# Kernel optimization log

Hardware: AMD Instinct MI355X
Metric: run time of the kernel (lower is better)

Reference implementation:

```python
import jax, jax.numpy as jnp
import numpy as np

N_HEAD = 16
N_BLOCKS = 2
EPS = 1e-6

def _rmsnorm(x, g):
    return x * jax.lax.rsqrt(jnp.mean(x * x, axis=-1, keepdims=True) + EPS) * g

def _causal_sa(x, Wqkv, Wproj, g):
    # x: (B, T, C); fused qkv, RMSNorm on q/k over full C before head split
    B, T, C = x.shape
    hd = C // N_HEAD
    q, k, v = jnp.split(x @ Wqkv, 3, axis=-1)
    q = _rmsnorm(q, g)
    k = _rmsnorm(k, g)
    def heads(t):
        return t.reshape(B, T, N_HEAD, hd).transpose(0, 2, 1, 3)
    q, k, v = heads(q), heads(k), heads(v)
    scores = jnp.einsum('bhqd,bhkd->bhqk', q, k) * (1.0 / np.sqrt(hd))
    mask = jnp.tril(jnp.ones((T, T), dtype=bool))
    scores = jnp.where(mask, scores, -jnp.finfo(scores.dtype).max)
    att = jax.nn.softmax(scores, axis=-1)
    y = jnp.einsum('bhqk,bhkd->bhqd', att, v)
    y = y.transpose(0, 2, 1, 3).reshape(B, T, C)
    return y @ Wproj

def setup_inputs() -> dict:
    key = jax.random.key(0)
    ks = jax.random.split(key, 8)
    B, ng, T, C = 2, 8, 256, 1024
    M_loc, M_glob = 16, 16
    s = 0.02
    return {
        'x': jax.random.normal(ks[0], (B, ng, T, C), jnp.float32),
        'mem_tokens': jax.random.normal(ks[1], (B, M_glob, C), jnp.float32),
        'local_mem': jax.random.normal(ks[2], (B, ng, M_loc, C), jnp.float32),
        'Wqkv_loc': jax.random.normal(ks[3], (N_BLOCKS, C, 3 * C), jnp.float32) * s,
        'Wproj_loc': jax.random.normal(ks[4], (N_BLOCKS, C, C), jnp.float32) * s,
        'g_loc': jnp.ones((N_BLOCKS, C), jnp.float32),
        'Wqkv_glob': jax.random.normal(ks[5], (N_BLOCKS, C, 3 * C), jnp.float32) * s,
        'Wproj_glob': jax.random.normal(ks[6], (N_BLOCKS, C, C), jnp.float32) * s,
        'g_glob': jnp.ones((N_BLOCKS, C), jnp.float32),
    }

def reference(x, mem_tokens, local_mem, Wqkv_loc, Wproj_loc, g_loc, Wqkv_glob, Wproj_glob, g_glob):
    B, ng, T, C = x.shape
    M_loc = local_mem.shape[2]
    M_glob = mem_tokens.shape[1]
    for i in range(N_BLOCKS):
        # local causal SA: per-group, with local mem tokens prepended
        xl = jnp.concatenate([local_mem, x], axis=2).reshape(B * ng, M_loc + T, C)
        yl = _causal_sa(xl, Wqkv_loc[i], Wproj_loc[i], g_loc[i])
        yl = yl.reshape(B, ng, M_loc + T, C)
        local_mem = yl[:, :, :M_loc, :]
        x = yl[:, :, M_loc:, :]
        # global causal SA over flattened sequence with global mem tokens
        xg = x.reshape(B, ng * T, C)
        xg = jnp.concatenate([mem_tokens, xg], axis=1)
        yg = _causal_sa(xg, Wqkv_glob[i], Wproj_glob[i], g_glob[i])
        mem_tokens = yg[:, :M_glob, :]
        x = yg[:, M_glob:, :].reshape(B, ng, T, C)
    return x
```

## Files before the change

kernel.cpp:

```cpp
#include <hip/hip_runtime.h>
#include <hip/hip_bf16.h>
#include <math.h>

typedef __attribute__((ext_vector_type(8))) short s16x8;
typedef __attribute__((ext_vector_type(4))) short s16x4;
typedef __attribute__((ext_vector_type(4))) float f32x4;

#define MPAD 4352
#define LG 2064
#define CT 8

__device__ __forceinline__ short f2b(float f) {
  unsigned u = __float_as_uint(f);
  unsigned r = (u + 0x7fffu + ((u >> 16) & 1u)) >> 16;
  return (short)(unsigned short)r;
}
__device__ __forceinline__ float b2f(short s) {
  return __uint_as_float(((unsigned)(unsigned short)s) << 16);
}

__device__ __forceinline__ void gl_lds16(const short* g, short* l) {
  __builtin_amdgcn_global_load_lds((const __attribute__((address_space(1))) short*)g,
                                   (__attribute__((address_space(3))) short*)l, 16, 0, 0);
}

__global__ __launch_bounds__(256) void transpose_cast(const float* __restrict__ in,
                                                      short* __restrict__ out,
                                                      int K, int N) {
  __shared__ float tile[32][33];
  int bn = blockIdx.x * 32;
  int bk = blockIdx.y * 32;
  for (int i = threadIdx.y; i < 32; i += 8)
    tile[i][threadIdx.x] = in[(size_t)(bk + i) * N + bn + threadIdx.x];
  __syncthreads();
  for (int i = threadIdx.y; i < 32; i += 8)
    out[(size_t)(bn + i) * K + bk + threadIdx.x] = f2b(tile[threadIdx.x][i]);
}

__global__ __launch_bounds__(256) void transpose_v(const short* __restrict__ QKV,
                                                   short* __restrict__ Vt,
                                                   int L, int Lpad) {
  __shared__ short tile[32][33];
  int sh = blockIdx.z;
  int s = sh >> 4, h = sh & 15;
  int kb = blockIdx.x * 32;
  int cb = blockIdx.y * 32;
  int tx = threadIdx.x;
  for (int i = threadIdx.y; i < 32; i += 8) {
    int key = kb + i;
    if (key > L - 1) key = L - 1;
    tile[i][tx] = QKV[(size_t)(s * L + key) * 3072 + 2048 + h * 64 + cb + tx];
  }
  __syncthreads();
  for (int i = threadIdx.y; i < 32; i += 8)
    Vt[((size_t)sh * 64 + cb + i) * Lpad + kb + tx] = tile[tx][i];
}

__global__ __launch_bounds__(256) void gemm_bt2(const short* __restrict__ A,
                                                const short* __restrict__ BT,
                                                short* __restrict__ C,
                                                int K, int N) {
  __shared__ short As[128 * 32];
  __shared__ short Bs[128 * 32];
  const int tid = threadIdx.x;
  const int lane = tid & 63;
  const int w = tid >> 6;
  const int wr = (w >> 1) * 64, wc = (w & 1) * 64;
  const int m0 = blockIdx.y * 128;
  const int n0 = blockIdx.x * 128;
  const int l15 = lane & 15, lhi = lane >> 4;

  f32x4 acc[4][4] = {};

  for (int k0 = 0; k0 < K; k0 += 32) {
    __syncthreads();
#pragma unroll
    for (int p = 0; p < 2; ++p) {
      int g = w * 128 + p * 64 + lane;
      int row = g >> 2;
      int cs = (g & 3) * 8;
      gl_lds16(A + (size_t)(m0 + row) * K + k0 + cs, &As[g * 8]);
      gl_lds16(BT + (size_t)(n0 + row) * K + k0 + cs, &Bs[g * 8]);
    }
    __syncthreads();
    s16x8 af[4], bf[4];
#pragma unroll
    for (int m = 0; m < 4; ++m)
      af[m] = *(const s16x8*)(&As[(wr + m * 16 + l15) * 32 + lhi * 8]);
#pragma unroll
    for (int n = 0; n < 4; ++n)
      bf[n] = *(const s16x8*)(&Bs[(wc + n * 16 + l15) * 32 + lhi * 8]);
#pragma unroll
    for (int m = 0; m < 4; ++m)
#pragma unroll
      for (int n = 0; n < 4; ++n)
        acc[m][n] = __builtin_amdgcn_mfma_f32_16x16x32_bf16(af[m], bf[n], acc[m][n], 0, 0, 0);
  }
#pragma unroll
  for (int m = 0; m < 4; ++m) {
    int row_base = m0 + wr + m * 16 + lhi * 4;
#pragma unroll
    for (int n = 0; n < 4; ++n) {
      int col = n0 + wc + n * 16 + l15;
#pragma unroll
      for (int r = 0; r < 4; ++r)
        C[(size_t)(row_base + r) * N + col] = f2b(acc[m][n][r]);
    }
  }
}

__global__ __launch_bounds__(256) void rmsnorm_qk(short* __restrict__ QKV,
                                                  const float* __restrict__ g) {
  int row = blockIdx.x;
  int which = blockIdx.y;
  size_t base = (size_t)row * 3072 + (size_t)which * 1024;
  int t = threadIdx.x;
  s16x4 in = *(const s16x4*)(QKV + base + t * 4);
  float v[4];
  float ss = 0.f;
#pragma unroll
  for (int j = 0; j < 4; ++j) {
    v[j] = b2f(in[j]);
    ss += v[j] * v[j];
  }
#pragma unroll
  for (int m = 32; m >= 1; m >>= 1) ss += __shfl_xor(ss, m);
  __shared__ float red[4];
  if ((t & 63) == 0) red[t >> 6] = ss;
  __syncthreads();
  float tot = red[0] + red[1] + red[2] + red[3];
  float inv = rsqrtf(tot * (1.0f / 1024.0f) + 1e-6f);
  if (which == 0) inv *= 0.125f;
  s16x4 out;
#pragma unroll
  for (int j = 0; j < 4; ++j) out[j] = f2b(v[j] * inv * g[t * 4 + j]);
  *(s16x4*)(&QKV[base + t * 4]) = out;
}

__global__ __launch_bounds__(256) void attn_causal3(const short* __restrict__ QKV,
                                                    const short* __restrict__ Vt,
                                                    short* __restrict__ Y,
                                                    int L, int Lpad) {
  const int h = blockIdx.y, s = blockIdx.z;
  const int q0 = blockIdx.x * 64;
  const int tid = threadIdx.x;
  const int lane = tid & 63, w = tid >> 6;
  const int l15 = lane & 15, lhi = lane >> 4;
  const int row0 = s * L;

  __shared__ short Ks[64][72];
  __shared__ short Vs[2][64][72];
  __shared__ short Ps[4][16][72];

  int qld = q0 + w * 16 + l15;
  if (qld > L - 1) qld = L - 1;
  const size_t qrow = (size_t)(row0 + qld) * 3072 + h * 64;
  s16x8 qf0 = *(const s16x8*)(QKV + qrow + lhi * 8);
  s16x8 qf1 = *(const s16x8*)(QKV + qrow + 32 + lhi * 8);

  float lsum[4] = {0.f, 0.f, 0.f, 0.f};
  f32x4 o[4];
#pragma unroll
  for (int d = 0; d < 4; ++d) o[d] = f32x4{0.f, 0.f, 0.f, 0.f};

  const short* Vbase = Vt + (size_t)(s * 16 + h) * 64 * Lpad;

  s16x8 kreg[2], vreg[2];
#pragma unroll
  for (int p = 0; p < 2; ++p) {
    int g = tid + p * 256;
    int kr = g >> 3, cs = (g & 7) * 8;
    int krow = kr;
    if (krow > L - 1) krow = L - 1;
    kreg[p] = *(const s16x8*)(QKV + (size_t)(row0 + krow) * 3072 + 1024 + h * 64 + cs);
    vreg[p] = *(const s16x8*)(Vbase + (size_t)kr * Lpad + cs);
  }

  int buf = 0;
  for (int kb = 0; kb <= q0; kb += 64, buf ^= 1) {
#pragma unroll
    for (int p = 0; p < 2; ++p) {
      int g = tid + p * 256;
      int kr = g >> 3, cs = (g & 7) * 8;
      *(s16x8*)(&Ks[kr][cs]) = kreg[p];
      *(s16x8*)(&Vs[buf][kr][cs]) = vreg[p];
    }
    if (kb + 64 <= q0) {
#pragma unroll
      for (int p = 0; p < 2; ++p) {
        int g = tid + p * 256;
        int kr = g >> 3, cs = (g & 7) * 8;
        int krow = kb + 64 + kr;
        if (krow > L - 1) krow = L - 1;
        kreg[p] = *(const s16x8*)(QKV + (size_t)(row0 + krow) * 3072 + 1024 + h * 64 + cs);
        vreg[p] = *(const s16x8*)(Vbase + (size_t)kr * Lpad + kb + 64 + cs);
      }
    }
    __syncthreads();

    f32x4 st[4];
#pragma unroll
    for (int n = 0; n < 4; ++n) {
      s16x8 k0 = *(const s16x8*)(&Ks[n * 16 + l15][lhi * 8]);
      s16x8 k1 = *(const s16x8*)(&Ks[n * 16 + l15][32 + lhi * 8]);
      f32x4 sa = f32x4{0.f, 0.f, 0.f, 0.f};
      sa = __builtin_amdgcn_mfma_f32_16x16x32_bf16(qf0, k0, sa, 0, 0, 0);
      sa = __builtin_amdgcn_mfma_f32_16x16x32_bf16(qf1, k1, sa, 0, 0, 0);
      st[n] = sa;
    }

    if (kb == q0) {
#pragma unroll
      for (int n = 0; n < 4; ++n) {
        int key = kb + n * 16 + l15;
#pragma unroll
        for (int r = 0; r < 4; ++r) {
          int qr = q0 + w * 16 + lhi * 4 + r;
          if (key > qr) st[n][r] = -1e30f;
        }
      }
    }

#pragma unroll
    for (int n = 0; n < 4; ++n) {
#pragma unroll
      for (int r = 0; r < 4; ++r) {
        float p = __expf(st[n][r] - 8.0f);
        Ps[w][lhi * 4 + r][n * 16 + l15] = f2b(p);
        lsum[r] += p;
      }
    }
    __syncthreads();

#pragma unroll
    for (int kk = 0; kk < 2; ++kk) {
      s16x8 pa = *(const s16x8*)(&Ps[w][l15][kk * 32 + lhi * 8]);
#pragma unroll
      for (int d = 0; d < 4; ++d) {
        s16x8 vf = *(const s16x8*)(&Vs[buf][d * 16 + l15][kk * 32 + lhi * 8]);
        o[d] = __builtin_amdgcn_mfma_f32_16x16x32_bf16(pa, vf, o[d], 0, 0, 0);
      }
    }
  }

#pragma unroll
  for (int r = 0; r < 4; ++r) {
#pragma unroll
    for (int mm = 1; mm <= 8; mm <<= 1) lsum[r] += __shfl_xor(lsum[r], mm, 16);
  }
#pragma unroll
  for (int d = 0; d < 4; ++d) {
#pragma unroll
    for (int r = 0; r < 4; ++r) {
      int qr = q0 + w * 16 + lhi * 4 + r;
      if (qr < L)
        Y[(size_t)(row0 + qr) * 1024 + h * 64 + d * 16 + l15] = f2b(o[d][r] / lsum[r]);
    }
  }
}

__global__ __launch_bounds__(256) void attn_split(const short* __restrict__ QKV,
                                                  const short* __restrict__ Vt,
                                                  float* __restrict__ o_acc,
                                                  float* __restrict__ ls_acc) {
  const int qb = blockIdx.x;
  const int chunk = blockIdx.y;
  const int sh = blockIdx.z;
  const int t0 = chunk * CT;
  if (t0 > qb) return;
  const int t1 = min(t0 + CT, qb + 1);
  const int h = sh & 15, s = sh >> 4;
  const int q0 = qb * 64;
  const int tid = threadIdx.x;
  const int lane = tid & 63, w = tid >> 6;
  const int l15 = lane & 15, lhi = lane >> 4;
  const int row0 = s * LG;
  const int Lpad = 2112;

  __shared__ short Ks[64][72];
  __shared__ short Vs[2][64][72];
  __shared__ short Ps[4][16][72];

  int qld = q0 + w * 16 + l15;
  if (qld > LG - 1) qld = LG - 1;
  const size_t qrow = (size_t)(row0 + qld) * 3072 + h * 64;
  s16x8 qf0 = *(const s16x8*)(QKV + qrow + lhi * 8);
  s16x8 qf1 = *(const s16x8*)(QKV + qrow + 32 + lhi * 8);

  float lsum[4] = {0.f, 0.f, 0.f, 0.f};
  f32x4 o[4];
#pragma unroll
  for (int d = 0; d < 4; ++d) o[d] = f32x4{0.f, 0.f, 0.f, 0.f};

  const short* Vbase = Vt + (size_t)sh * 64 * Lpad;

  s16x8 kreg[2], vreg[2];
  const int kb0 = t0 * 64;
#pragma unroll
  for (int p = 0; p < 2; ++p) {
    int g = tid + p * 256;
    int kr = g >> 3, cs = (g & 7) * 8;
    int krow = kb0 + kr;
    if (krow > LG - 1) krow = LG - 1;
    kreg[p] = *(const s16x8*)(QKV + (size_t)(row0 + krow) * 3072 + 1024 + h * 64 + cs);
    vreg[p] = *(const s16x8*)(Vbase + (size_t)kr * Lpad + kb0 + cs);
  }

  int buf = 0;
  for (int t = t0; t < t1; ++t, buf ^= 1) {
    const int kb = t * 64;
#pragma unroll
    for (int p = 0; p < 2; ++p) {
      int g = tid + p * 256;
      int kr = g >> 3, cs = (g & 7) * 8;
      *(s16x8*)(&Ks[kr][cs]) = kreg[p];
      *(s16x8*)(&Vs[buf][kr][cs]) = vreg[p];
    }
    if (t + 1 < t1) {
#pragma unroll
      for (int p = 0; p < 2; ++p) {
        int g = tid + p * 256;
        int kr = g >> 3, cs = (g & 7) * 8;
        int krow = kb + 64 + kr;
        if (krow > LG - 1) krow = LG - 1;
        kreg[p] = *(const s16x8*)(QKV + (size_t)(row0 + krow) * 3072 + 1024 + h * 64 + cs);
        vreg[p] = *(const s16x8*)(Vbase + (size_t)kr * Lpad + kb + 64 + cs);
      }
    }
    __syncthreads();

    f32x4 st[4];
#pragma unroll
    for (int n = 0; n < 4; ++n) {
      s16x8 k0 = *(const s16x8*)(&Ks[n * 16 + l15][lhi * 8]);
      s16x8 k1 = *(const s16x8*)(&Ks[n * 16 + l15][32 + lhi * 8]);
      f32x4 sa = f32x4{0.f, 0.f, 0.f, 0.f};
      sa = __builtin_amdgcn_mfma_f32_16x16x32_bf16(qf0, k0, sa, 0, 0, 0);
      sa = __builtin_amdgcn_mfma_f32_16x16x32_bf16(qf1, k1, sa, 0, 0, 0);
      st[n] = sa;
    }

    if (t == qb) {
#pragma unroll
      for (int n = 0; n < 4; ++n) {
        int key = kb + n * 16 + l15;
#pragma unroll
        for (int r = 0; r < 4; ++r) {
          int qr = q0 + w * 16 + lhi * 4 + r;
          if (key > qr) st[n][r] = -1e30f;
        }
      }
    }

#pragma unroll
    for (int n = 0; n < 4; ++n) {
#pragma unroll
      for (int r = 0; r < 4; ++r) {
        float p = __expf(st[n][r] - 8.0f);
        Ps[w][lhi * 4 + r][n * 16 + l15] = f2b(p);
        lsum[r] += p;
      }
    }
    __syncthreads();

#pragma unroll
    for (int kk = 0; kk < 2; ++kk) {
      s16x8 pa = *(const s16x8*)(&Ps[w][l15][kk * 32 + lhi * 8]);
#pragma unroll
      for (int d = 0; d < 4; ++d) {
        s16x8 vf = *(const s16x8*)(&Vs[buf][d * 16 + l15][kk * 32 + lhi * 8]);
        o[d] = __builtin_amdgcn_mfma_f32_16x16x32_bf16(pa, vf, o[d], 0, 0, 0);
      }
    }
  }

#pragma unroll
  for (int r = 0; r < 4; ++r) {
#pragma unroll
    for (int mm = 1; mm <= 8; mm <<= 1) lsum[r] += __shfl_xor(lsum[r], mm, 16);
  }
#pragma unroll
  for (int r = 0; r < 4; ++r) {
    int qr = q0 + w * 16 + lhi * 4 + r;
    if (qr < LG) {
      if (l15 == 0) atomicAdd(&ls_acc[(size_t)sh * LG + qr], lsum[r]);
#pragma unroll
      for (int d = 0; d < 4; ++d)
        atomicAdd(&o_acc[((size_t)sh * LG + qr) * 64 + d * 16 + l15], o[d][r]);
    }
  }
}

__global__ __launch_bounds__(256) void attn_merge(const float* __restrict__ o_acc,
                                                  const float* __restrict__ ls_acc,
                                                  short* __restrict__ Y) {
  int sh = blockIdx.z * 16 + blockIdx.y;
  int s = sh >> 4, h = sh & 15;
  int row = blockIdx.x * 4 + (threadIdx.x >> 6);
  int col = threadIdx.x & 63;
  if (row < LG) {
    float inv = 1.0f / ls_acc[(size_t)sh * LG + row];
    float v = o_acc[((size_t)sh * LG + row) * 64 + col];
    Y[(size_t)(s * LG + row) * 1024 + h * 64 + col] = f2b(v * inv);
  }
}

__global__ __launch_bounds__(256) void build_xl(const float* __restrict__ x,
                                                const float* __restrict__ lm,
                                                short* __restrict__ Xin) {
  int row = blockIdx.x;
  int s = row / 272, r = row % 272;
  const float* src = (r < 16) ? lm + ((size_t)s * 16 + r) * 1024
                              : x + ((size_t)s * 256 + (r - 16)) * 1024;
  int t = threadIdx.x;
  f32x4 v = *(const f32x4*)(src + t * 4);
  s16x4 o;
#pragma unroll
  for (int j = 0; j < 4; ++j) o[j] = f2b(v[j]);
  *(s16x4*)(&Xin[(size_t)row * 1024 + t * 4]) = o;
}

__global__ __launch_bounds__(256) void build_xg(const float* __restrict__ x,
                                                const float* __restrict__ mem,
                                                short* __restrict__ Xin) {
  int row = blockIdx.x;
  int sr = row < 4128 ? row : 4127;
  int b = sr / 2064, r = sr % 2064;
  const float* src = (r < 16) ? mem + ((size_t)b * 16 + r) * 1024
                              : x + ((size_t)b * 2048 + (r - 16)) * 1024;
  int t = threadIdx.x;
  f32x4 v = *(const f32x4*)(src + t * 4);
  s16x4 o;
#pragma unroll
  for (int j = 0; j < 4; ++j) o[j] = f2b(v[j]);
  *(s16x4*)(&Xin[(size_t)row * 1024 + t * 4]) = o;
}

__global__ __launch_bounds__(256) void split_local(const short* __restrict__ Pout,
                                                   float* __restrict__ x,
                                                   float* __restrict__ lm) {
  int row = blockIdx.x;
  int s = row / 272, r = row % 272;
  int t = threadIdx.x;
  s16x4 v = *(const s16x4*)(Pout + (size_t)row * 1024 + t * 4);
  float* dst = (r < 16) ? lm + ((size_t)s * 16 + r) * 1024
                        : x + ((size_t)s * 256 + (r - 16)) * 1024;
  f32x4 o;
#pragma unroll
  for (int j = 0; j < 4; ++j) o[j] = b2f(v[j]);
  *(f32x4*)(dst + t * 4) = o;
}

__global__ __launch_bounds__(256) void split_global(const short* __restrict__ Pout,
                                                    float* __restrict__ x,
                                                    float* __restrict__ mem) {
  int row = blockIdx.x;
  int b = row / 2064, r = row % 2064;
  int t = threadIdx.x;
  s16x4 v = *(const s16x4*)(Pout + (size_t)row * 1024 + t * 4);
  float* dst = (r < 16) ? mem + ((size_t)b * 16 + r) * 1024
                        : x + ((size_t)b * 2048 + (r - 16)) * 1024;
  f32x4 o;
#pragma unroll
  for (int j = 0; j < 4; ++j) o[j] = b2f(v[j]);
  *(f32x4*)(dst + t * 4) = o;
}

extern "C" void kernel_launch(void* const* d_in, const int* in_sizes, int n_in,
                              void* d_out, int out_size, void* d_ws, size_t ws_size,
                              hipStream_t stream) {
  const float* x_in = (const float*)d_in[0];
  const float* mem_in = (const float*)d_in[1];
  const float* lm_in = (const float*)d_in[2];
  const float* Wqkv_loc = (const float*)d_in[3];
  const float* Wproj_loc = (const float*)d_in[4];
  const float* g_loc = (const float*)d_in[5];
  const float* Wqkv_glob = (const float*)d_in[6];
  const float* Wproj_glob = (const float*)d_in[7];
  const float* g_glob = (const float*)d_in[8];

  char* ws = (char*)d_ws;
  size_t off = 0;
  auto alloc = [&](size_t bytes) {
    char* p = ws + off;
    off += (bytes + 255) & ~(size_t)255;
    return p;
  };
  short* Wt = (short*)alloc((size_t)3072 * 1024 * 2);
  float* x_cur = (float*)alloc((size_t)4096 * 1024 * 4);
  float* lm_cur = (float*)alloc((size_t)256 * 1024 * 4);
  float* mem_cur = (float*)alloc((size_t)32 * 1024 * 4);
  short* Xin = (short*)alloc((size_t)MPAD * 1024 * 2);
  short* QKVb = (short*)alloc((size_t)MPAD * 3072 * 2);
  short* Yb = (short*)alloc((size_t)MPAD * 1024 * 2);
  short* Pout = (short*)alloc((size_t)MPAD * 1024 * 2);
  short* Vtb = (short*)alloc((size_t)256 * 64 * 320 * 2);
  size_t oacc_bytes = (size_t)32 * LG * 64 * 4;
  size_t lacc_bytes = (size_t)32 * LG * 4;
  float* o_acc = (float*)alloc(oacc_bytes);
  float* ls_acc = (float*)alloc(lacc_bytes);
  const bool use_split = (ws_size >= off);

  hipMemcpyAsync(x_cur, x_in, (size_t)4096 * 1024 * 4, hipMemcpyDeviceToDevice, stream);
  hipMemcpyAsync(lm_cur, lm_in, (size_t)256 * 1024 * 4, hipMemcpyDeviceToDevice, stream);
  hipMemcpyAsync(mem_cur, mem_in, (size_t)32 * 1024 * 4, hipMemcpyDeviceToDevice, stream);

  for (int i = 0; i < 2; ++i) {
    transpose_cast<<<dim3(96, 32), dim3(32, 8), 0, stream>>>(
        Wqkv_loc + (size_t)i * 1024 * 3072, Wt, 1024, 3072);
    build_xl<<<4352, 256, 0, stream>>>(x_cur, lm_cur, Xin);
    gemm_bt2<<<dim3(24, 34), 256, 0, stream>>>(Xin, Wt, QKVb, 1024, 3072);
    rmsnorm_qk<<<dim3(4352, 2), 256, 0, stream>>>(QKVb, g_loc + (size_t)i * 1024);
    transpose_v<<<dim3(10, 2, 256), dim3(32, 8), 0, stream>>>(QKVb, Vtb, 272, 320);
    attn_causal3<<<dim3(5, 16, 16), 256, 0, stream>>>(QKVb, Vtb, Yb, 272, 320);
    transpose_cast<<<dim3(32, 32), dim3(32, 8), 0, stream>>>(
        Wproj_loc + (size_t)i * 1024 * 1024, Wt, 1024, 1024);
    gemm_bt2<<<dim3(8, 34), 256, 0, stream>>>(Yb, Wt, Pout, 1024, 1024);
    split_local<<<4352, 256, 0, stream>>>(Pout, x_cur, lm_cur);

    transpose_cast<<<dim3(96, 32), dim3(32, 8), 0, stream>>>(
        Wqkv_glob + (size_t)i * 1024 * 3072, Wt, 1024, 3072);
    build_xg<<<4352, 256, 0, stream>>>(x_cur, mem_cur, Xin);
    gemm_bt2<<<dim3(24, 34), 256, 0, stream>>>(Xin, Wt, QKVb, 1024, 3072);
    rmsnorm_qk<<<dim3(4128, 2), 256, 0, stream>>>(QKVb, g_glob + (size_t)i * 1024);
    transpose_v<<<dim3(66, 2, 32), dim3(32, 8), 0, stream>>>(QKVb, Vtb, 2064, 2112);
    if (use_split) {
      hipMemsetAsync(o_acc, 0, oacc_bytes, stream);
      hipMemsetAsync(ls_acc, 0, lacc_bytes, stream);
      attn_split<<<dim3(33, 5, 32), 256, 0, stream>>>(QKVb, Vtb, o_acc, ls_acc);
      attn_merge<<<dim3(516, 16, 2), 256, 0, stream>>>(o_acc, ls_acc, Yb);
    } else {
      attn_causal3<<<dim3(33, 16, 2), 256, 0, stream>>>(QKVb, Vtb, Yb, 2064, 2112);
    }
    transpose_cast<<<dim3(32, 32), dim3(32, 8), 0, stream>>>(
        Wproj_glob + (size_t)i * 1024 * 1024, Wt, 1024, 1024);
    gemm_bt2<<<dim3(8, 34), 256, 0, stream>>>(Yb, Wt, Pout, 1024, 1024);
    split_global<<<4128, 256, 0, stream>>>(Pout, x_cur, mem_cur);
  }

  hipMemcpyAsync(d_out, x_cur, (size_t)4096 * 1024 * 4, hipMemcpyDeviceToDevice, stream);
}
```

Measured before the change: 655.8 us.

## Double-buffer GEMM staging, fuse split/build kernels, switch softmax to exp2

The GEMM now double-buffers its LDS tiles, loading the next K-slice while MFMAs consume the current one, with one barrier per iteration instead of two. The split and build kernels are merged so projection output is copied straight into the next stage's bf16 input, which removes the fp32 x_cur round trip and the device-to-device memcpys. Softmax folds log2(e) into the q scaling and uses exp2f with an equivalent shift. The cost is doubled GEMM LDS use, which may lower occupancy, and the fusion adds extra index arithmetic.

```diff
diff --git a/kernel.cpp b/kernel.cpp
--- a/kernel.cpp
+++ b/kernel.cpp
@@ -9,6 +9,7 @@
 #define MPAD 4352
 #define LG 2064
 #define CT 8
+#define SM_SHIFT 11.5415603f
 
 __device__ __forceinline__ short f2b(float f) {
   unsigned u = __float_as_uint(f);
@@ -56,12 +57,12 @@
     Vt[((size_t)sh * 64 + cb + i) * Lpad + kb + tx] = tile[tx][i];
 }
 
-__global__ __launch_bounds__(256) void gemm_bt2(const short* __restrict__ A,
+__global__ __launch_bounds__(256) void gemm_bt3(const short* __restrict__ A,
                                                 const short* __restrict__ BT,
                                                 short* __restrict__ C,
                                                 int K, int N) {
-  __shared__ short As[128 * 32];
-  __shared__ short Bs[128 * 32];
+  __shared__ short As[2][128 * 32];
+  __shared__ short Bs[2][128 * 32];
   const int tid = threadIdx.x;
   const int lane = tid & 63;
   const int w = tid >> 6;
@@ -72,29 +73,37 @@
 
   f32x4 acc[4][4] = {};
 
-  for (int k0 = 0; k0 < K; k0 += 32) {
-    __syncthreads();
+  auto STAGE = [&](int b, int k0) {
 #pragma unroll
     for (int p = 0; p < 2; ++p) {
       int g = w * 128 + p * 64 + lane;
       int row = g >> 2;
       int cs = (g & 3) * 8;
-      gl_lds16(A + (size_t)(m0 + row) * K + k0 + cs, &As[g * 8]);
-      gl_lds16(BT + (size_t)(n0 + row) * K + k0 + cs, &Bs[g * 8]);
-    }
-    __syncthreads();
+      gl_lds16(A + (size_t)(m0 + row) * K + k0 + cs, &As[b][g * 8]);
+      gl_lds16(BT + (size_t)(n0 + row) * K + k0 + cs, &Bs[b][g * 8]);
+    }
+  };
+
+  const int nt = K >> 5;
+  STAGE(0, 0);
+  __syncthreads();
+  int cur = 0;
+  for (int t = 0; t < nt; ++t) {
+    if (t + 1 < nt) STAGE(cur ^ 1, (t + 1) << 5);
     s16x8 af[4], bf[4];
 #pragma unroll
     for (int m = 0; m < 4; ++m)
-      af[m] = *(const s16x8*)(&As[(wr + m * 16 + l15) * 32 + lhi * 8]);
+      af[m] = *(const s16x8*)(&As[cur][(wr + m * 16 + l15) * 32 + lhi * 8]);
 #pragma unroll
     for (int n = 0; n < 4; ++n)
-      bf[n] = *(const s16x8*)(&Bs[(wc + n * 16 + l15) * 32 + lhi * 8]);
+      bf[n] = *(const s16x8*)(&Bs[cur][(wc + n * 16 + l15) * 32 + lhi * 8]);
 #pragma unroll
     for (int m = 0; m < 4; ++m)
 #pragma unroll
       for (int n = 0; n < 4; ++n)
         acc[m][n] = __builtin_amdgcn_mfma_f32_16x16x32_bf16(af[m], bf[n], acc[m][n], 0, 0, 0);
+    __syncthreads();
+    cur ^= 1;
   }
 #pragma unroll
   for (int m = 0; m < 4; ++m) {
@@ -130,7 +139,7 @@
   __syncthreads();
   float tot = red[0] + red[1] + red[2] + red[3];
   float inv = rsqrtf(tot * (1.0f / 1024.0f) + 1e-6f);
-  if (which == 0) inv *= 0.125f;
+  if (which == 0) inv *= 0.125f * 1.44269504f;
   s16x4 out;
 #pragma unroll
   for (int j = 0; j < 4; ++j) out[j] = f2b(v[j] * inv * g[t * 4 + j]);
@@ -225,7 +234,7 @@
     for (int n = 0; n < 4; ++n) {
 #pragma unroll
       for (int r = 0; r < 4; ++r) {
-        float p = __expf(st[n][r] - 8.0f);
+        float p = exp2f(st[n][r] - SM_SHIFT);
         Ps[w][lhi * 4 + r][n * 16 + l15] = f2b(p);
         lsum[r] += p;
       }
@@ -356,7 +365,7 @@
     for (int n = 0; n < 4; ++n) {
 #pragma unroll
       for (int r = 0; r < 4; ++r) {
-        float p = __expf(st[n][r] - 8.0f);
+        float p = exp2f(st[n][r] - SM_SHIFT);
         Ps[w][lhi * 4 + r][n * 16 + l15] = f2b(p);
         lsum[r] += p;
       }
@@ -420,50 +429,77 @@
   *(s16x4*)(&Xin[(size_t)row * 1024 + t * 4]) = o;
 }
 
-__global__ __launch_bounds__(256) void build_xg(const float* __restrict__ x,
-                                                const float* __restrict__ mem,
-                                                short* __restrict__ Xin) {
+__global__ __launch_bounds__(256) void split_local_build_xg(const short* __restrict__ Pout,
+                                                            const float* __restrict__ mem_src,
+                                                            float* __restrict__ lm_out,
+                                                            short* __restrict__ Xin) {
   int row = blockIdx.x;
-  int sr = row < 4128 ? row : 4127;
-  int b = sr / 2064, r = sr % 2064;
-  const float* src = (r < 16) ? mem + ((size_t)b * 16 + r) * 1024
-                              : x + ((size_t)b * 2048 + (r - 16)) * 1024;
   int t = threadIdx.x;
-  f32x4 v = *(const f32x4*)(src + t * 4);
-  s16x4 o;
-#pragma unroll
-  for (int j = 0; j < 4; ++j) o[j] = f2b(v[j]);
-  *(s16x4*)(&Xin[(size_t)row * 1024 + t * 4]) = o;
-}
-
-__global__ __launch_bounds__(256) void split_local(const short* __restrict__ Pout,
-                                                   float* __restrict__ x,
-                                                   float* __restrict__ lm) {
+  if (row < 4352) {
+    int sr = row < 4128 ? row : 4127;
+    int b = sr / 2064, r = sr % 2064;
+    s16x4 o;
+    if (r < 16) {
+      f32x4 v = *(const f32x4*)(mem_src + ((size_t)(b * 16 + r)) * 1024 + t * 4);
+#pragma unroll
+      for (int j = 0; j < 4; ++j) o[j] = f2b(v[j]);
+    } else {
+      int f = b * 2048 + (r - 16);
+      int pr = (f >> 8) * 272 + 16 + (f & 255);
+      o = *(const s16x4*)(Pout + (size_t)pr * 1024 + t * 4);
+    }
+    *(s16x4*)(&Xin[(size_t)row * 1024 + t * 4]) = o;
+  } else {
+    int m = row - 4352;
+    int pr = (m >> 4) * 272 + (m & 15);
+    s16x4 v = *(const s16x4*)(Pout + (size_t)pr * 1024 + t * 4);
+    f32x4 o;
+#pragma unroll
+    for (int j = 0; j < 4; ++j) o[j] = b2f(v[j]);
+    *(f32x4*)(&lm_out[(size_t)m * 1024 + t * 4]) = o;
+  }
+}
+
+__global__ __launch_bounds__(256) void split_global_build_xl(const short* __restrict__ Pout,
+                                                             const float* __restrict__ lm_src,
+                                                             float* __restrict__ mem_out,
+                                                             short* __restrict__ Xin) {
   int row = blockIdx.x;
-  int s = row / 272, r = row % 272;
   int t = threadIdx.x;
-  s16x4 v = *(const s16x4*)(Pout + (size_t)row * 1024 + t * 4);
-  float* dst = (r < 16) ? lm + ((size_t)s * 16 + r) * 1024
-                        : x + ((size_t)s * 256 + (r - 16)) * 1024;
+  if (row < 4352) {
+    int s = row / 272, r = row % 272;
+    s16x4 o;
+    if (r < 16) {
+      f32x4 v = *(const f32x4*)(lm_src + ((size_t)(s * 16 + r)) * 1024 + t * 4);
+#pragma unroll
+      for (int j = 0; j < 4; ++j) o[j] = f2b(v[j]);
+    } else {
+      int f = s * 256 + (r - 16);
+      int pr = (f >> 11) * 2064 + 16 + (f & 2047);
+      o = *(const s16x4*)(Pout + (size_t)pr * 1024 + t * 4);
+    }
+    *(s16x4*)(&Xin[(size_t)row * 1024 + t * 4]) = o;
+  } else {
+    int m = row - 4352;
+    int pr = (m >> 4) * 2064 + (m & 15);
+    s16x4 v = *(const s16x4*)(Pout + (size_t)pr * 1024 + t * 4);
+    f32x4 o;
+#pragma unroll
+    for (int j = 0; j < 4; ++j) o[j] = b2f(v[j]);
+    *(f32x4*)(&mem_out[(size_t)m * 1024 + t * 4]) = o;
+  }
+}
+
+__global__ __launch_bounds__(256) void split_global_final(const short* __restrict__ Pout,
+                                                          float* __restrict__ out) {
+  int f = blockIdx.x;
+  int t = threadIdx.x;
+  int pr = (f >> 11) * 2064 + 16 + (f & 2047);
+  s16x4 v = *(const s16x4*)(Pout + (size_t)pr * 1024 + t * 4);
   f32x4 o;
 #pragma unroll
   for (int j = 0; j < 4; ++j) o[j] = b2f(v[j]);
-  *(f32x4*)(dst + t * 4) = o;
-}
-
-__global__ __launch_bounds__(256) void split_global(const short* __restrict__ Pout,
-                                                    float* __restrict__ x,
-                                                    float* __restrict__ mem) {
-  int row = blockIdx.x;
-  int b = row / 2064, r = row % 2064;
-  int t = threadIdx.x;
-  s16x4 v = *(const s16x4*)(Pout + (size_t)row * 1024 + t * 4);
-  float* dst = (r < 16) ? mem + ((size_t)b * 16 + r) * 1024
-                        : x + ((size_t)b * 2048 + (r - 16)) * 1024;
-  f32x4 o;
-#pragma unroll
-  for (int j = 0; j < 4; ++j) o[j] = b2f(v[j]);
-  *(f32x4*)(dst + t * 4) = o;
+  *(f32x4*)(&out[(size_t)f * 1024 + t * 4]) = o;
 }
 
 extern "C" void kernel_launch(void* const* d_in, const int* in_sizes, int n_in,
@@ -487,7 +523,6 @@
     return p;
   };
   short* Wt = (short*)alloc((size_t)3072 * 1024 * 2);
-  float* x_cur = (float*)alloc((size_t)4096 * 1024 * 4);
   float* lm_cur = (float*)alloc((size_t)256 * 1024 * 4);
   float* mem_cur = (float*)alloc((size_t)32 * 1024 * 4);
   short* Xin = (short*)alloc((size_t)MPAD * 1024 * 2);
@@ -501,27 +536,23 @@
   float* ls_acc = (float*)alloc(lacc_bytes);
   const bool use_split = (ws_size >= off);
 
-  hipMemcpyAsync(x_cur, x_in, (size_t)4096 * 1024 * 4, hipMemcpyDeviceToDevice, stream);
-  hipMemcpyAsync(lm_cur, lm_in, (size_t)256 * 1024 * 4, hipMemcpyDeviceToDevice, stream);
-  hipMemcpyAsync(mem_cur, mem_in, (size_t)32 * 1024 * 4, hipMemcpyDeviceToDevice, stream);
-
   for (int i = 0; i < 2; ++i) {
     transpose_cast<<<dim3(96, 32), dim3(32, 8), 0, stream>>>(
         Wqkv_loc + (size_t)i * 1024 * 3072, Wt, 1024, 3072);
-    build_xl<<<4352, 256, 0, stream>>>(x_cur, lm_cur, Xin);
-    gemm_bt2<<<dim3(24, 34), 256, 0, stream>>>(Xin, Wt, QKVb, 1024, 3072);
+    if (i == 0) build_xl<<<4352, 256, 0, stream>>>(x_in, lm_in, Xin);
+    gemm_bt3<<<dim3(24, 34), 256, 0, stream>>>(Xin, Wt, QKVb, 1024, 3072);
     rmsnorm_qk<<<dim3(4352, 2), 256, 0, stream>>>(QKVb, g_loc + (size_t)i * 1024);
     transpose_v<<<dim3(10, 2, 256), dim3(32, 8), 0, stream>>>(QKVb, Vtb, 272, 320);
     attn_causal3<<<dim3(5, 16, 16), 256, 0, stream>>>(QKVb, Vtb, Yb, 272, 320);
     transpose_cast<<<dim3(32, 32), dim3(32, 8), 0, stream>>>(
         Wproj_loc + (size_t)i * 1024 * 1024, Wt, 1024, 1024);
-    gemm_bt2<<<dim3(8, 34), 256, 0, stream>>>(Yb, Wt, Pout, 1024, 1024);
-    split_local<<<4352, 256, 0, stream>>>(Pout, x_cur, lm_cur);
+    gemm_bt3<<<dim3(8, 34), 256, 0, stream>>>(Yb, Wt, Pout, 1024, 1024);
+    split_local_build_xg<<<4608, 256, 0, stream>>>(Pout, i == 0 ? mem_in : mem_cur,
+                                                   lm_cur, Xin);
 
     transpose_cast<<<dim3(96, 32), dim3(32, 8), 0, stream>>>(
         Wqkv_glob + (size_t)i * 1024 * 3072, Wt, 1024, 3072);
-    build_xg<<<4352, 256, 0, stream>>>(x_cur, mem_cur, Xin);
-    gemm_bt2<<<dim3(24, 34), 256, 0, stream>>>(Xin, Wt, QKVb, 1024, 3072);
+    gemm_bt3<<<dim3(24, 34), 256, 0, stream>>>(Xin, Wt, QKVb, 1024, 3072);
     rmsnorm_qk<<<dim3(4128, 2), 256, 0, stream>>>(QKVb, g_glob + (size_t)i * 1024);
     transpose_v<<<dim3(66, 2, 32), dim3(32, 8), 0, stream>>>(QKVb, Vtb, 2064, 2112);
     if (use_split) {
@@ -534,9 +565,10 @@
     }
     transpose_cast<<<dim3(32, 32), dim3(32, 8), 0, stream>>>(
         Wproj_glob + (size_t)i * 1024 * 1024, Wt, 1024, 1024);
-    gemm_bt2<<<dim3(8, 34), 256, 0, stream>>>(Yb, Wt, Pout, 1024, 1024);
-    split_global<<<4128, 256, 0, stream>>>(Pout, x_cur, mem_cur);
-  }
-
-  hipMemcpyAsync(d_out, x_cur, (size_t)4096 * 1024 * 4, hipMemcpyDeviceToDevice, stream);
-}
+    gemm_bt3<<<dim3(8, 34), 256, 0, stream>>>(Yb, Wt, Pout, 1024, 1024);
+    if (i == 0)
+      split_global_build_xl<<<4384, 256, 0, stream>>>(Pout, lm_cur, mem_cur, Xin);
+    else
+      split_global_final<<<4096, 256, 0, stream>>>(Pout, (float*)d_out);
+  }
+}
```

Result: faster. 605.8 us (-7.6%).
